# Optimization experiments

Hardware: AMD Instinct MI355X
Metric: run time of the kernel (lower is better)

The kernel has to match this reference:

```python
import jax, jax.numpy as jnp
import numpy as np

DIM = 256
NUM_HEADS = 8
CHUNK = 64
EPS = 1e-5


def layernorm(x, g, b):
    m = jnp.mean(x, axis=-1, keepdims=True)
    v = jnp.mean((x - m) ** 2, axis=-1, keepdims=True)
    return (x - m) / jnp.sqrt(v + EPS) * g + b


def setup_inputs() -> dict:
    key = jax.random.key(0)
    ks = jax.random.split(key, 12)
    B, C, H, W = 8, DIM, 64, 64
    s = 1.0 / np.sqrt(C)
    return {
        "x": jax.random.normal(ks[0], (B, C, H, W), jnp.float32),
        "CVA_input": jax.random.normal(ks[1], (B, C, H, W), jnp.float32),
        "qn_g": jnp.ones((C,), jnp.float32), "qn_b": jnp.zeros((C,), jnp.float32),
        "kn_g": jnp.ones((C,), jnp.float32), "kn_b": jnp.zeros((C,), jnp.float32),
        "vn_g": jnp.ones((C,), jnp.float32), "vn_b": jnp.zeros((C,), jnp.float32),
        "Wq": jax.random.normal(ks[2], (C, C), jnp.float32) * s,
        "bq": jnp.zeros((C,), jnp.float32),
        "Wk": jax.random.normal(ks[3], (C, C), jnp.float32) * s,
        "bk": jnp.zeros((C,), jnp.float32),
        "Wv": jax.random.normal(ks[4], (C, C), jnp.float32) * s,
        "bv": jnp.zeros((C,), jnp.float32),
        "Wp": jax.random.normal(ks[5], (C, C), jnp.float32) * s,
        "bp": jnp.zeros((C,), jnp.float32),
    }


def reference(x, CVA_input, qn_g, qn_b, kn_g, kn_b, vn_g, vn_b,
              Wq, bq, Wk, bk, Wv, bv, Wp, bp):
    B, C, H, W = x.shape
    N = H * W
    nh = NUM_HEADS
    hd = C // nh
    scale = hd ** -0.5
    nc = N // CHUNK  # number of non-overlapping chunks

    xs = x.reshape(B, C, N).transpose(0, 2, 1)          # [B,N,C]
    cva = CVA_input.reshape(B, -1, C)                    # [B,N,C] (raw reshape, as in torch)

    def heads(t):  # [B,N,C] -> [B,nh,nc,CHUNK,hd]
        return t.reshape(B, N, nh, hd).transpose(0, 2, 1, 3).reshape(B, nh, nc, CHUNK, hd)

    q = heads(layernorm(cva, qn_g, qn_b) @ Wq + bq)
    k = heads(layernorm(cva, kn_g, kn_b) @ Wk + bk)
    v = heads(layernorm(xs, vn_g, vn_b) @ Wv + bv)

    # block-local attention: each chunk attends only within itself
    scores = jnp.einsum('bhncd,bhnkd->bhnck', q, k) * scale  # [B,nh,nc,CHUNK,CHUNK]
    probs = jax.nn.softmax(scores, axis=-1)
    o = jnp.einsum('bhnck,bhnkd->bhncd', probs, v)           # [B,nh,nc,CHUNK,hd]

    o = o.reshape(B, nh, N, hd).transpose(0, 2, 1, 3).reshape(B, N, C)
    out = o @ Wp + bp                                        # [B,N,C]
    return out.transpose(0, 2, 1).reshape(B, C, H, W)
```

## Files before the change

kernel.cpp:

```cpp
#include <hip/hip_runtime.h>
#include <hip/hip_bf16.h>

#define NTOK 4096
#define BATCH 8
#define NROWS (BATCH * NTOK)

typedef __attribute__((ext_vector_type(8))) short bfx8;
typedef __attribute__((ext_vector_type(4))) short bfx4;
typedef __attribute__((ext_vector_type(4))) float f32x4;

__device__ __forceinline__ short f2bf(float f) {
    unsigned u = __builtin_bit_cast(unsigned, f);
    u += 0x7fffu + ((u >> 16) & 1u);
    return (short)(u >> 16);
}
__device__ __forceinline__ unsigned pk2(float a, float b) {
    return (unsigned)(unsigned short)f2bf(a) | ((unsigned)(unsigned short)f2bf(b) << 16);
}

#define MFMA16(a, b, c) __builtin_amdgcn_mfma_f32_16x16x32_bf16(a, b, c, 0, 0, 0)
#define LGKM0()                                              \
    do {                                                     \
        asm volatile("s_waitcnt lgkmcnt(0)" ::: "memory");   \
        __builtin_amdgcn_sched_barrier(0);                   \
    } while (0)

__global__ __launch_bounds__(256) void prep_w(
    const float* __restrict__ Wq, const float* __restrict__ Wk,
    const float* __restrict__ Wv, const float* __restrict__ Wp,
    const float* __restrict__ qg, const float* __restrict__ qb,
    const float* __restrict__ kg, const float* __restrict__ kb,
    const float* __restrict__ vg, const float* __restrict__ vb,
    short* __restrict__ wt, float* __restrict__ bbp) {
    int m = blockIdx.x;
    int ci0 = blockIdx.y * 16;
    const float *W, *g, *be;
    float scale = 1.0f;
    if (m == 0)      { W = Wq; g = qg; be = qb; scale = 0.17677669529663687f; }
    else if (m == 1) { W = Wk; g = kg; be = kb; }
    else if (m == 2) { W = Wv; g = vg; be = vb; }
    else             { W = Wp; g = nullptr; be = nullptr; }
    __shared__ float tile[16][257];
    int t = threadIdx.x;
#pragma unroll
    for (int i = 0; i < 16; i++)
        tile[i][t] = W[(size_t)(ci0 + i) * 256 + t];
    __syncthreads();
    float p = 0.f;
    if (be) {
#pragma unroll
        for (int i = 0; i < 16; i++) p += be[ci0 + i] * tile[i][t];
    }
    bbp[(m * 16 + blockIdx.y) * 256 + t] = p;
    short* WT = wt + m * 65536 + t * 256 + ci0;
    bfx8 o0, o1;
#pragma unroll
    for (int j = 0; j < 8; j++) {
        float gv = g ? g[ci0 + j] : 1.0f;
        o0[j] = f2bf(scale * gv * tile[j][t]);
    }
#pragma unroll
    for (int j = 0; j < 8; j++) {
        float gv = g ? g[ci0 + 8 + j] : 1.0f;
        o1[j] = f2bf(scale * gv * tile[8 + j][t]);
    }
    *reinterpret_cast<bfx8*>(WT) = o0;
    *reinterpret_cast<bfx8*>(WT + 8) = o1;
}

__global__ __launch_bounds__(256) void prep_b(
    const float* __restrict__ bq, const float* __restrict__ bk,
    const float* __restrict__ bv, const float* __restrict__ bp,
    const float* __restrict__ bbp, float* __restrict__ bb) {
    int m = blockIdx.x, t = threadIdx.x;
    const float* bias = (m == 0) ? bq : (m == 1) ? bk : (m == 2) ? bv : bp;
    float scale = (m == 0) ? 0.17677669529663687f : 1.0f;
    float s = bias[t];
#pragma unroll
    for (int i = 0; i < 16; i++) s += bbp[(m * 16 + i) * 256 + t];
    bb[m * 256 + t] = scale * s;
}

__global__ __launch_bounds__(512, 4) void mega(const float* __restrict__ x,
                                               const float* __restrict__ cva,
                                               const short* __restrict__ wt,
                                               const float* __restrict__ bb,
                                               float* __restrict__ out) {
    int id = blockIdx.x;
    int b = id >> 6, ch = id & 63;
    int t = threadIdx.x, w = t >> 6, l = t & 63, c = l & 15, g = l >> 4;

    __shared__ short A[64 * 264];
    __shared__ short scr_[8][2560];
    __shared__ float red[8][64][2];
    short* S = scr_[w];

    const float* xb   = x + (size_t)b * 1048576 + ch * 64;
    const float* cvab = cva + (size_t)(b * 4096 + ch * 64) * 256;

#pragma unroll
    for (int i = 0; i < 8; i++) {
        int row = w * 8 + i;
        float4 v = *reinterpret_cast<const float4*>(cvab + (size_t)row * 256 + l * 4);
        float s = v.x + v.y + v.z + v.w;
        float q2 = v.x * v.x + v.y * v.y + v.z * v.z + v.w * v.w;
#pragma unroll
        for (int m = 1; m < 64; m <<= 1) { s += __shfl_xor(s, m); q2 += __shfl_xor(q2, m); }
        float mean = s * (1.0f / 256.0f);
        float rstd = rsqrtf(q2 * (1.0f / 256.0f) - mean * mean + 1e-5f);
        bfx4 o;
        o[0] = f2bf((v.x - mean) * rstd);
        o[1] = f2bf((v.y - mean) * rstd);
        o[2] = f2bf((v.z - mean) * rstd);
        o[3] = f2bf((v.w - mean) * rstd);
        *reinterpret_cast<bfx4*>(A + row * 264 + l * 4) = o;
    }
    __syncthreads();

    f32x4 qa[4][2] = {};
    {
        const short* w0 = wt + (size_t)(w * 32 + c) * 256 + g * 8;
        const short* w1 = w0 + 16 * 256;
#pragma unroll
        for (int ks = 0; ks < 8; ks++) {
            bfx8 af[4];
#pragma unroll
            for (int m = 0; m < 4; m++)
                af[m] = *reinterpret_cast<const bfx8*>(A + (m * 16 + c) * 264 + ks * 32 + g * 8);
            bfx8 q0 = *reinterpret_cast<const bfx8*>(w0 + ks * 32);
            bfx8 q1 = *reinterpret_cast<const bfx8*>(w1 + ks * 32);
#pragma unroll
            for (int m = 0; m < 4; m++) {
                qa[m][0] = MFMA16(af[m], q0, qa[m][0]);
                qa[m][1] = MFMA16(af[m], q1, qa[m][1]);
            }
        }
    }
    bfx8 qf[4];
    {
        float b0 = bb[w * 32 + c], b1 = bb[w * 32 + 16 + c];
#pragma unroll
        for (int m = 0; m < 4; m++)
#pragma unroll
            for (int j = 0; j < 4; j++) {
                S[(m * 16 + g * 4 + j) * 40 + c]      = f2bf(qa[m][0][j] + b0);
                S[(m * 16 + g * 4 + j) * 40 + 16 + c] = f2bf(qa[m][1][j] + b1);
            }
        LGKM0();
#pragma unroll
        for (int np = 0; np < 4; np++)
            qf[np] = *reinterpret_cast<const bfx8*>(S + (np * 16 + c) * 40 + g * 8);
        LGKM0();
    }

    f32x4 ka[4][2] = {};
    {
        const short* w0 = wt + 65536 + (size_t)(w * 32 + c) * 256 + g * 8;
        const short* w1 = w0 + 16 * 256;
#pragma unroll
        for (int ks = 0; ks < 8; ks++) {
            bfx8 af[4];
#pragma unroll
            for (int m = 0; m < 4; m++)
                af[m] = *reinterpret_cast<const bfx8*>(A + (m * 16 + c) * 264 + ks * 32 + g * 8);
            bfx8 k0 = *reinterpret_cast<const bfx8*>(w0 + ks * 32);
            bfx8 k1 = *reinterpret_cast<const bfx8*>(w1 + ks * 32);
#pragma unroll
            for (int m = 0; m < 4; m++) {
                ka[m][0] = MFMA16(af[m], k0, ka[m][0]);
                ka[m][1] = MFMA16(af[m], k1, ka[m][1]);
            }
        }
    }

    float xg[32];
#pragma unroll
    for (int i = 0; i < 32; i++) xg[i] = xb[(size_t)(w * 32 + i) * 4096 + l];

    bfx8 kf[4];
    {
        float b0 = bb[256 + w * 32 + c], b1 = bb[256 + w * 32 + 16 + c];
#pragma unroll
        for (int m = 0; m < 4; m++)
#pragma unroll
            for (int j = 0; j < 4; j++) {
                S[(m * 16 + g * 4 + j) * 40 + c]      = f2bf(ka[m][0][j] + b0);
                S[(m * 16 + g * 4 + j) * 40 + 16 + c] = f2bf(ka[m][1][j] + b1);
            }
        LGKM0();
#pragma unroll
        for (int m = 0; m < 4; m++)
            kf[m] = *reinterpret_cast<const bfx8*>(S + (m * 16 + c) * 40 + g * 8);
        LGKM0();
    }

    {
        float s = 0.f, q2 = 0.f;
#pragma unroll
        for (int i = 0; i < 32; i++) { s += xg[i]; q2 += xg[i] * xg[i]; }
        red[w][l][0] = s;
        red[w][l][1] = q2;
    }
    __syncthreads();

    float xmean, xrstd;
    {
        float s = 0.f, q2 = 0.f;
#pragma unroll
        for (int j2 = 0; j2 < 8; j2++) { s += red[j2][l][0]; q2 += red[j2][l][1]; }
        xmean = s * (1.0f / 256.0f);
        xrstd = rsqrtf(q2 * (1.0f / 256.0f) - xmean * xmean + 1e-5f);
    }

#pragma unroll
    for (int i2 = 0; i2 < 4; i2++) {
        bfx8 o;
#pragma unroll
        for (int jj = 0; jj < 8; jj++) o[jj] = f2bf((xg[i2 * 8 + jj] - xmean) * xrstd);
        *reinterpret_cast<bfx8*>(A + l * 264 + w * 32 + i2 * 8) = o;
    }
    __syncthreads();

    f32x4 sa[4][4] = {};
#pragma unroll
    for (int m = 0; m < 4; m++)
#pragma unroll
        for (int np = 0; np < 4; np++)
            sa[m][np] = MFMA16(kf[m], qf[np], sa[m][np]);

    float rs[4];
#pragma unroll
    for (int np = 0; np < 4; np++) {
        float mx = sa[0][np][0];
#pragma unroll
        for (int m = 0; m < 4; m++)
#pragma unroll
            for (int j = 0; j < 4; j++) mx = fmaxf(mx, sa[m][np][j]);
        mx = fmaxf(mx, __shfl_xor(mx, 16));
        mx = fmaxf(mx, __shfl_xor(mx, 32));
        float sum = 0.f;
#pragma unroll
        for (int m = 0; m < 4; m++)
#pragma unroll
            for (int j = 0; j < 4; j++) {
                float e = __expf(sa[m][np][j] - mx);
                sa[m][np][j] = e;
                sum += e;
            }
        sum += __shfl_xor(sum, 16);
        sum += __shfl_xor(sum, 32);
        rs[np] = 1.0f / sum;
    }

    unsigned Pp[4][4][2];
#pragma unroll
    for (int m = 0; m < 4; m++)
#pragma unroll
        for (int np = 0; np < 4; np++) {
            Pp[m][np][0] = pk2(sa[m][np][0], sa[m][np][1]);
            Pp[m][np][1] = pk2(sa[m][np][2], sa[m][np][3]);
        }

    f32x4 va[4][2] = {};
    {
        const short* w0 = wt + 2 * 65536 + (size_t)(w * 32 + c) * 256 + g * 8;
        const short* w1 = w0 + 16 * 256;
#pragma unroll
        for (int ks = 0; ks < 8; ks++) {
            bfx8 af[4];
#pragma unroll
            for (int m = 0; m < 4; m++)
                af[m] = *reinterpret_cast<const bfx8*>(A + (m * 16 + c) * 264 + ks * 32 + g * 8);
            bfx8 v0 = *reinterpret_cast<const bfx8*>(w0 + ks * 32);
            bfx8 v1 = *reinterpret_cast<const bfx8*>(w1 + ks * 32);
#pragma unroll
            for (int m = 0; m < 4; m++) {
                va[m][0] = MFMA16(af[m], v0, va[m][0]);
                va[m][1] = MFMA16(af[m], v1, va[m][1]);
            }
        }
    }
    __syncthreads();

    bfx8 vf[2][2];
    {
        float b0 = bb[512 + w * 32 + c], b1 = bb[512 + w * 32 + 16 + c];
#pragma unroll
        for (int m = 0; m < 4; m++)
#pragma unroll
            for (int j = 0; j < 4; j++) {
                S[c * 72 + m * 16 + g * 4 + j]        = f2bf(va[m][0][j] + b0);
                S[(16 + c) * 72 + m * 16 + g * 4 + j] = f2bf(va[m][1][j] + b1);
            }
        LGKM0();
#pragma unroll
        for (int ks = 0; ks < 2; ks++)
#pragma unroll
            for (int mD = 0; mD < 2; mD++)
                vf[ks][mD] = *reinterpret_cast<const bfx8*>(S + (mD * 16 + c) * 72 + ks * 32 + g * 8);
        LGKM0();
    }

    f32x4 oa[2][4] = {};
#pragma unroll
    for (int ks = 0; ks < 2; ks++) {
#pragma unroll
        for (int m2 = 0; m2 < 2; m2++)
#pragma unroll
            for (int np = 0; np < 4; np++) {
                *reinterpret_cast<unsigned*>(S + (np * 16 + c) * 40 + m2 * 16 + g * 4)     = Pp[ks * 2 + m2][np][0];
                *reinterpret_cast<unsigned*>(S + (np * 16 + c) * 40 + m2 * 16 + g * 4 + 2) = Pp[ks * 2 + m2][np][1];
            }
        LGKM0();
        bfx8 pf[4];
#pragma unroll
        for (int np = 0; np < 4; np++)
            pf[np] = *reinterpret_cast<const bfx8*>(S + (np * 16 + c) * 40 + g * 8);
        LGKM0();
#pragma unroll
        for (int mD = 0; mD < 2; mD++)
#pragma unroll
            for (int np = 0; np < 4; np++)
                oa[mD][np] = MFMA16(vf[ks][mD], pf[np], oa[mD][np]);
    }

#pragma unroll
    for (int mD = 0; mD < 2; mD++)
#pragma unroll
        for (int np = 0; np < 4; np++) {
            bfx4 o4;
#pragma unroll
            for (int j = 0; j < 4; j++) o4[j] = f2bf(oa[mD][np][j] * rs[np]);
            *reinterpret_cast<bfx4*>(A + (np * 16 + c) * 264 + w * 32 + mD * 16 + g * 4) = o4;
        }
    __syncthreads();

    {
        f32x4 pa[4][2] = {};
        const short* w0 = wt + 3 * 65536 + (size_t)(w * 32 + c) * 256 + g * 8;
        const short* w1 = w0 + 16 * 256;
#pragma unroll
        for (int ks = 0; ks < 8; ks++) {
            bfx8 af[4];
#pragma unroll
            for (int m = 0; m < 4; m++)
                af[m] = *reinterpret_cast<const bfx8*>(A + (m * 16 + c) * 264 + ks * 32 + g * 8);
            bfx8 p0 = *reinterpret_cast<const bfx8*>(w0 + ks * 32);
            bfx8 p1 = *reinterpret_cast<const bfx8*>(w1 + ks * 32);
#pragma unroll
            for (int m = 0; m < 4; m++) {
                pa[m][0] = MFMA16(af[m], p0, pa[m][0]);
                pa[m][1] = MFMA16(af[m], p1, pa[m][1]);
            }
        }
        float* trw = reinterpret_cast<float*>(S);
        float* outb = out + (size_t)b * 1048576 + ch * 64;
#pragma unroll
        for (int p = 0; p < 2; p++) {
            float bvv = bb[768 + w * 32 + p * 16 + c];
#pragma unroll
            for (int m = 0; m < 4; m++)
#pragma unroll
                for (int j = 0; j < 4; j++)
                    trw[c * 65 + m * 16 + g * 4 + j] = pa[m][p][j] + bvv;
            LGKM0();
#pragma unroll
            for (int cl = 0; cl < 16; cl++) {
                int co = w * 32 + p * 16 + cl;
                outb[(size_t)co * 4096 + l] = trw[cl * 65 + l];
            }
            LGKM0();
        }
    }
}

extern "C" void kernel_launch(void* const* d_in, const int* in_sizes, int n_in,
                              void* d_out, int out_size, void* d_ws, size_t ws_size,
                              hipStream_t stream) {
    const float* x   = (const float*)d_in[0];
    const float* cva = (const float*)d_in[1];
    const float* qg  = (const float*)d_in[2];
    const float* qb  = (const float*)d_in[3];
    const float* kg  = (const float*)d_in[4];
    const float* kb  = (const float*)d_in[5];
    const float* vg  = (const float*)d_in[6];
    const float* vb  = (const float*)d_in[7];
    const float* Wq  = (const float*)d_in[8];
    const float* bq  = (const float*)d_in[9];
    const float* Wk  = (const float*)d_in[10];
    const float* bk  = (const float*)d_in[11];
    const float* Wv  = (const float*)d_in[12];
    const float* bv  = (const float*)d_in[13];
    const float* Wp  = (const float*)d_in[14];
    const float* bp  = (const float*)d_in[15];
    float* out = (float*)d_out;
    char* ws = (char*)d_ws;

    short* wt  = (short*)(ws);
    float* bb  = (float*)(ws + 4 * 65536 * sizeof(short));
    float* bbp = bb + 1024;

    prep_w<<<dim3(4, 16), 256, 0, stream>>>(Wq, Wk, Wv, Wp, qg, qb, kg, kb, vg, vb,
                                            wt, bbp);
    prep_b<<<4, 256, 0, stream>>>(bq, bk, bv, bp, bbp, bb);

    mega<<<512, 512, 0, stream>>>(x, cva, wt, bb, out);
}
```

Measured before the change: 67.76 us.

## Fuse Q/K projection loops, hoist x loads and V GEMM, vectorize V stores

Merges the separate Q and K projection GEMMs into one loop that reuses the same A-fragment LDS reads, and batches the cva row loads before the layernorm math. The x gather is moved earlier and the V projection is moved ahead of the score/softmax MFMAs, so global loads and independent MFMA work can overlap. The V-tile transpose writes to scratch now go out as 4-wide stores instead of scalar ones. These changes raise register pressure (16 accumulators live at once plus 32 prefetched floats), which could cause spills at the 512x4 launch bound.

```diff
diff --git a/kernel.cpp b/kernel.cpp
--- a/kernel.cpp
+++ b/kernel.cpp
@@ -98,44 +98,61 @@
     const float* xb   = x + (size_t)b * 1048576 + ch * 64;
     const float* cvab = cva + (size_t)(b * 4096 + ch * 64) * 256;
 
-#pragma unroll
-    for (int i = 0; i < 8; i++) {
-        int row = w * 8 + i;
-        float4 v = *reinterpret_cast<const float4*>(cvab + (size_t)row * 256 + l * 4);
-        float s = v.x + v.y + v.z + v.w;
-        float q2 = v.x * v.x + v.y * v.y + v.z * v.z + v.w * v.w;
-#pragma unroll
-        for (int m = 1; m < 64; m <<= 1) { s += __shfl_xor(s, m); q2 += __shfl_xor(q2, m); }
-        float mean = s * (1.0f / 256.0f);
-        float rstd = rsqrtf(q2 * (1.0f / 256.0f) - mean * mean + 1e-5f);
-        bfx4 o;
-        o[0] = f2bf((v.x - mean) * rstd);
-        o[1] = f2bf((v.y - mean) * rstd);
-        o[2] = f2bf((v.z - mean) * rstd);
-        o[3] = f2bf((v.w - mean) * rstd);
-        *reinterpret_cast<bfx4*>(A + row * 264 + l * 4) = o;
-    }
-    __syncthreads();
-
-    f32x4 qa[4][2] = {};
-    {
-        const short* w0 = wt + (size_t)(w * 32 + c) * 256 + g * 8;
-        const short* w1 = w0 + 16 * 256;
+    {
+        float4 vv[8];
+#pragma unroll
+        for (int i = 0; i < 8; i++)
+            vv[i] = *reinterpret_cast<const float4*>(cvab + (size_t)(w * 8 + i) * 256 + l * 4);
+#pragma unroll
+        for (int i = 0; i < 8; i++) {
+            int row = w * 8 + i;
+            float4 v = vv[i];
+            float s = v.x + v.y + v.z + v.w;
+            float q2 = v.x * v.x + v.y * v.y + v.z * v.z + v.w * v.w;
+#pragma unroll
+            for (int m = 1; m < 64; m <<= 1) { s += __shfl_xor(s, m); q2 += __shfl_xor(q2, m); }
+            float mean = s * (1.0f / 256.0f);
+            float rstd = rsqrtf(q2 * (1.0f / 256.0f) - mean * mean + 1e-5f);
+            bfx4 o;
+            o[0] = f2bf((v.x - mean) * rstd);
+            o[1] = f2bf((v.y - mean) * rstd);
+            o[2] = f2bf((v.z - mean) * rstd);
+            o[3] = f2bf((v.w - mean) * rstd);
+            *reinterpret_cast<bfx4*>(A + row * 264 + l * 4) = o;
+        }
+    }
+    __syncthreads();
+
+    f32x4 qa[4][2] = {}, ka[4][2] = {};
+    {
+        const short* wq0 = wt + (size_t)(w * 32 + c) * 256 + g * 8;
+        const short* wq1 = wq0 + 16 * 256;
+        const short* wk0 = wq0 + 65536;
+        const short* wk1 = wq1 + 65536;
 #pragma unroll
         for (int ks = 0; ks < 8; ks++) {
             bfx8 af[4];
 #pragma unroll
             for (int m = 0; m < 4; m++)
                 af[m] = *reinterpret_cast<const bfx8*>(A + (m * 16 + c) * 264 + ks * 32 + g * 8);
-            bfx8 q0 = *reinterpret_cast<const bfx8*>(w0 + ks * 32);
-            bfx8 q1 = *reinterpret_cast<const bfx8*>(w1 + ks * 32);
+            bfx8 q0 = *reinterpret_cast<const bfx8*>(wq0 + ks * 32);
+            bfx8 q1 = *reinterpret_cast<const bfx8*>(wq1 + ks * 32);
+            bfx8 k0 = *reinterpret_cast<const bfx8*>(wk0 + ks * 32);
+            bfx8 k1 = *reinterpret_cast<const bfx8*>(wk1 + ks * 32);
 #pragma unroll
             for (int m = 0; m < 4; m++) {
                 qa[m][0] = MFMA16(af[m], q0, qa[m][0]);
                 qa[m][1] = MFMA16(af[m], q1, qa[m][1]);
-            }
-        }
-    }
+                ka[m][0] = MFMA16(af[m], k0, ka[m][0]);
+                ka[m][1] = MFMA16(af[m], k1, ka[m][1]);
+            }
+        }
+    }
+
+    float xg[32];
+#pragma unroll
+    for (int i = 0; i < 32; i++) xg[i] = xb[(size_t)(w * 32 + i) * 4096 + l];
+
     bfx8 qf[4];
     {
         float b0 = bb[w * 32 + c], b1 = bb[w * 32 + 16 + c];
@@ -153,30 +170,6 @@
         LGKM0();
     }
 
-    f32x4 ka[4][2] = {};
-    {
-        const short* w0 = wt + 65536 + (size_t)(w * 32 + c) * 256 + g * 8;
-        const short* w1 = w0 + 16 * 256;
-#pragma unroll
-        for (int ks = 0; ks < 8; ks++) {
-            bfx8 af[4];
-#pragma unroll
-            for (int m = 0; m < 4; m++)
-                af[m] = *reinterpret_cast<const bfx8*>(A + (m * 16 + c) * 264 + ks * 32 + g * 8);
-            bfx8 k0 = *reinterpret_cast<const bfx8*>(w0 + ks * 32);
-            bfx8 k1 = *reinterpret_cast<const bfx8*>(w1 + ks * 32);
-#pragma unroll
-            for (int m = 0; m < 4; m++) {
-                ka[m][0] = MFMA16(af[m], k0, ka[m][0]);
-                ka[m][1] = MFMA16(af[m], k1, ka[m][1]);
-            }
-        }
-    }
-
-    float xg[32];
-#pragma unroll
-    for (int i = 0; i < 32; i++) xg[i] = xb[(size_t)(w * 32 + i) * 4096 + l];
-
     bfx8 kf[4];
     {
         float b0 = bb[256 + w * 32 + c], b1 = bb[256 + w * 32 + 16 + c];
@@ -220,6 +213,26 @@
         *reinterpret_cast<bfx8*>(A + l * 264 + w * 32 + i2 * 8) = o;
     }
     __syncthreads();
+
+    f32x4 va[4][2] = {};
+    {
+        const short* w0 = wt + 2 * 65536 + (size_t)(w * 32 + c) * 256 + g * 8;
+        const short* w1 = w0 + 16 * 256;
+#pragma unroll
+        for (int ks = 0; ks < 8; ks++) {
+            bfx8 af[4];
+#pragma unroll
+            for (int m = 0; m < 4; m++)
+                af[m] = *reinterpret_cast<const bfx8*>(A + (m * 16 + c) * 264 + ks * 32 + g * 8);
+            bfx8 v0 = *reinterpret_cast<const bfx8*>(w0 + ks * 32);
+            bfx8 v1 = *reinterpret_cast<const bfx8*>(w1 + ks * 32);
+#pragma unroll
+            for (int m = 0; m < 4; m++) {
+                va[m][0] = MFMA16(af[m], v0, va[m][0]);
+                va[m][1] = MFMA16(af[m], v1, va[m][1]);
+            }
+        }
+    }
 
     f32x4 sa[4][4] = {};
 #pragma unroll
@@ -260,38 +273,22 @@
             Pp[m][np][0] = pk2(sa[m][np][0], sa[m][np][1]);
             Pp[m][np][1] = pk2(sa[m][np][2], sa[m][np][3]);
         }
-
-    f32x4 va[4][2] = {};
-    {
-        const short* w0 = wt + 2 * 65536 + (size_t)(w * 32 + c) * 256 + g * 8;
-        const short* w1 = w0 + 16 * 256;
-#pragma unroll
-        for (int ks = 0; ks < 8; ks++) {
-            bfx8 af[4];
-#pragma unroll
-            for (int m = 0; m < 4; m++)
-                af[m] = *reinterpret_cast<const bfx8*>(A + (m * 16 + c) * 264 + ks * 32 + g * 8);
-            bfx8 v0 = *reinterpret_cast<const bfx8*>(w0 + ks * 32);
-            bfx8 v1 = *reinterpret_cast<const bfx8*>(w1 + ks * 32);
-#pragma unroll
-            for (int m = 0; m < 4; m++) {
-                va[m][0] = MFMA16(af[m], v0, va[m][0]);
-                va[m][1] = MFMA16(af[m], v1, va[m][1]);
-            }
-        }
-    }
     __syncthreads();
 
     bfx8 vf[2][2];
     {
         float b0 = bb[512 + w * 32 + c], b1 = bb[512 + w * 32 + 16 + c];
 #pragma unroll
-        for (int m = 0; m < 4; m++)
+        for (int m = 0; m < 4; m++) {
+            bfx4 t0, t1;
 #pragma unroll
             for (int j = 0; j < 4; j++) {
-                S[c * 72 + m * 16 + g * 4 + j]        = f2bf(va[m][0][j] + b0);
-                S[(16 + c) * 72 + m * 16 + g * 4 + j] = f2bf(va[m][1][j] + b1);
-            }
+                t0[j] = f2bf(va[m][0][j] + b0);
+                t1[j] = f2bf(va[m][1][j] + b1);
+            }
+            *reinterpret_cast<bfx4*>(S + c * 72 + m * 16 + g * 4)        = t0;
+            *reinterpret_cast<bfx4*>(S + (16 + c) * 72 + m * 16 + g * 4) = t1;
+        }
         LGKM0();
 #pragma unroll
         for (int ks = 0; ks < 2; ks++)
```

Result: slower. 70.92 us (+4.7%).
